# Optimization experiments

Hardware: AMD Instinct MI355X
Metric: run time of the kernel (lower is better)

The kernel has to match this reference:

```python
import jax, jax.numpy as jnp
import numpy as np

D_MODEL = 1024
HEADS = 16
D_K = D_MODEL // HEADS
NEG_INF = -1e10


def setup_inputs() -> dict:
    key = jax.random.key(0)
    ks = jax.random.split(key, 10)
    n, s = 2, 2048
    inp = {
        "value": jax.random.normal(ks[0], (n, s, D_MODEL), dtype=jnp.float32),
        "key": jax.random.normal(ks[1], (n, s, D_MODEL), dtype=jnp.float32),
        "query": jax.random.normal(ks[2], (n, s, D_MODEL), dtype=jnp.float32),
        "mask": jax.random.randint(ks[3], (n, 1, s, s), 0, 2, dtype=jnp.int32),
        # torch.nn.Linear weights are [out, in]; y = x @ W.T (+ b)
        "Wq": jax.random.normal(ks[4], (D_MODEL, D_MODEL), dtype=jnp.float32) * (D_MODEL ** -0.5),
        "Wk": jax.random.normal(ks[5], (D_MODEL, D_MODEL), dtype=jnp.float32) * (D_MODEL ** -0.5),
        "Wv": jax.random.normal(ks[6], (D_MODEL, D_MODEL), dtype=jnp.float32) * (D_MODEL ** -0.5),
        "Wo": jax.random.normal(ks[7], (D_MODEL, D_MODEL), dtype=jnp.float32) * (D_MODEL ** -0.5),
        "bo": jax.random.normal(ks[8], (D_MODEL,), dtype=jnp.float32) * 0.01,
    }
    return inp


def reference(value, key, query, mask, Wq, Wk, Wv, Wo, bo):
    n, q_len, _ = query.shape
    # projections (Linear, no bias): x @ W.T
    q = (query @ Wq.T).reshape(n, q_len, HEADS, D_K)
    k = (key @ Wk.T).reshape(n, key.shape[1], HEADS, D_K)
    v = (value @ Wv.T).reshape(n, value.shape[1], HEADS, D_K)
    scores = jnp.einsum('nqhd,nkhd->nhqk', q, k)  # [n,h,q,k]
    scores = jnp.where(mask == 0, jnp.float32(NEG_INF), scores)
    attn = jax.nn.softmax(scores / jnp.sqrt(jnp.float32(D_K)), axis=-1)
    out = jnp.einsum('nhql,nlhd->nqhd', attn, v).reshape(n, q_len, D_MODEL)
    return out @ Wo.T + bo
```

## Files before the change

kernel.cpp:

```cpp
#include <hip/hip_runtime.h>
#include <hip/hip_bf16.h>
#include <stdint.h>

#define SEQ     2048
#define NBATCH  2
#define DMODEL  1024
#define NH      16
#define DKH     64

typedef __bf16 bf16;
typedef __attribute__((ext_vector_type(8))) __bf16 bf16x8;
typedef __attribute__((ext_vector_type(4))) __bf16 bf16x4;
typedef __attribute__((ext_vector_type(4))) float  f32x4;

static __device__ __forceinline__ f32x4 mfma16(bf16x8 a, bf16x8 b, f32x4 c) {
    return __builtin_amdgcn_mfma_f32_16x16x32_bf16(a, b, c, 0, 0, 0);
}

#define PL32SWAP(a, b) asm("v_permlane32_swap_b32 %0, %1" : "+v"(a), "+v"(b))
#define PL16SWAP(a, b) asm("v_permlane16_swap_b32 %0, %1" : "+v"(a), "+v"(b))

__global__ __launch_bounds__(256) void cvt_all_k(const float* __restrict__ q,
                                                 const float* __restrict__ k,
                                                 const float* __restrict__ v,
                                                 const float* __restrict__ wq,
                                                 const float* __restrict__ wk,
                                                 const float* __restrict__ wv,
                                                 const float* __restrict__ wo,
                                                 const int* __restrict__ mask,
                                                 bf16* __restrict__ qb, bf16* __restrict__ kb,
                                                 bf16* __restrict__ vb, bf16* __restrict__ wqb,
                                                 bf16* __restrict__ wkb, bf16* __restrict__ wvb,
                                                 bf16* __restrict__ wob,
                                                 unsigned long long* __restrict__ mbits) {
    if (blockIdx.y == 7) {
        const int nwords = NBATCH * SEQ * (SEQ / 64);
        int wave  = (blockIdx.x * blockDim.x + threadIdx.x) >> 6;
        int lane  = threadIdx.x & 63;
        int nwtot = (gridDim.x * blockDim.x) >> 6;
        for (int w = wave; w < nwords; w += nwtot) {
            int m = mask[(size_t)w * 64 + lane];
            unsigned long long b = __ballot(m != 0);
            if (lane == 0) mbits[w] = b;
        }
        return;
    }
    const float* src; bf16* dst; int n4;
    const int NX4 = (NBATCH * SEQ * DMODEL) / 4, NW4 = (DMODEL * DMODEL) / 4;
    switch (blockIdx.y) {
        case 0: src = q;  dst = qb;  n4 = NX4; break;
        case 1: src = k;  dst = kb;  n4 = NX4; break;
        case 2: src = v;  dst = vb;  n4 = NX4; break;
        case 3: src = wq; dst = wqb; n4 = NW4; break;
        case 4: src = wk; dst = wkb; n4 = NW4; break;
        case 5: src = wv; dst = wvb; n4 = NW4; break;
        default: src = wo; dst = wob; n4 = NW4; break;
    }
    int stride = gridDim.x * blockDim.x;
    for (int i = blockIdx.x * blockDim.x + threadIdx.x; i < n4; i += stride) {
        f32x4 f = ((const f32x4*)src)[i];
        bf16x4 o;
#pragma unroll
        for (int j = 0; j < 4; j++) o[j] = (bf16)f[j];
        ((bf16x4*)dst)[i] = o;
    }
}

__global__ __launch_bounds__(256) void qkv_gemm(const bf16* __restrict__ Xq,
                                                const bf16* __restrict__ Xk,
                                                const bf16* __restrict__ Xv,
                                                const bf16* __restrict__ Wq,
                                                const bf16* __restrict__ Wk,
                                                const bf16* __restrict__ Wv,
                                                bf16* __restrict__ Qo,
                                                bf16* __restrict__ Ko,
                                                bf16* __restrict__ Vto) {
    __shared__ bf16 As[128 * 32], Bs[128 * 32];
    const int z = blockIdx.z;
    const bf16* A = (z == 0) ? Xq : (z == 1) ? Xk : Xv;
    const bf16* W = (z == 0) ? Wq : (z == 1) ? Wk : Wv;
    const int bm = blockIdx.x * 128, bn = blockIdx.y * 128;
    const int tid = threadIdx.x, wave = tid >> 6, lane = tid & 63;
    const int wm = wave >> 1, wn = wave & 1, lo = lane & 15, hi = lane >> 4;

    const int r0 = wave * 32 + (lane >> 2);
    const int c8 = (lane & 3) * 8;
    const bf16* Ag = A + (size_t)(bm + r0) * DMODEL + c8;
    const bf16* Bg = W + (size_t)(bn + r0) * DMODEL + c8;
    bf16* lA = &As[wave * 1024 + (lane >> 2) * 32 + (lane & 3) * 8];
    bf16* lB = &Bs[wave * 1024 + (lane >> 2) * 32 + (lane & 3) * 8];

    f32x4 acc[4][4];
#pragma unroll
    for (int i = 0; i < 4; i++)
#pragma unroll
        for (int j = 0; j < 4; j++) acc[i][j] = 0.0f;

    bf16x8 ra0 = *(const bf16x8*)(Ag);
    bf16x8 ra1 = *(const bf16x8*)(Ag + (size_t)16 * DMODEL);
    bf16x8 rb0 = *(const bf16x8*)(Bg);
    bf16x8 rb1 = *(const bf16x8*)(Bg + (size_t)16 * DMODEL);

#pragma unroll 1
    for (int k0 = 0; k0 < DMODEL; k0 += 32) {
        __syncthreads();
        *(bf16x8*)lA         = ra0;
        *(bf16x8*)(lA + 512) = ra1;
        *(bf16x8*)lB         = rb0;
        *(bf16x8*)(lB + 512) = rb1;
        if (k0 + 32 < DMODEL) {
            ra0 = *(const bf16x8*)(Ag + k0 + 32);
            ra1 = *(const bf16x8*)(Ag + k0 + 32 + (size_t)16 * DMODEL);
            rb0 = *(const bf16x8*)(Bg + k0 + 32);
            rb1 = *(const bf16x8*)(Bg + k0 + 32 + (size_t)16 * DMODEL);
        }
        __syncthreads();

        bf16x8 a[4], b[4];
#pragma unroll
        for (int t = 0; t < 4; t++) {
            a[t] = *(const bf16x8*)&As[(wm * 64 + t * 16 + lo) * 32 + hi * 8];
            b[t] = *(const bf16x8*)&Bs[(wn * 64 + t * 16 + lo) * 32 + hi * 8];
        }
        if (z < 2) {
#pragma unroll
            for (int tm = 0; tm < 4; tm++)
#pragma unroll
                for (int tn = 0; tn < 4; tn++)
                    acc[tm][tn] = mfma16(a[tm], b[tn], acc[tm][tn]);
        } else {
#pragma unroll
            for (int tm = 0; tm < 4; tm++)
#pragma unroll
                for (int tn = 0; tn < 4; tn++)
                    acc[tm][tn] = mfma16(b[tn], a[tm], acc[tm][tn]);
        }
    }

    if (z < 2) {
        bf16* O = (z == 0) ? Qo : Ko;
        const float qscale = (z == 0) ? 0.18033688f : 1.0f;
#pragma unroll
        for (int tm = 0; tm < 4; tm++)
#pragma unroll
            for (int tn = 0; tn < 4; tn++)
#pragma unroll
                for (int r = 0; r < 4; r++) {
                    int m = bm + wm * 64 + tm * 16 + hi * 4 + r;
                    int o = bn + wn * 64 + tn * 16 + lo;
                    int nidx = m >> 11, sq = m & 2047;
                    int hh = o >> 6, d = o & 63;
                    O[(((size_t)nidx * NH + hh) * SEQ + sq) * DKH + d] = (bf16)(acc[tm][tn][r] * qscale);
                }
    } else {
#pragma unroll
        for (int tm = 0; tm < 4; tm++)
#pragma unroll
            for (int tn = 0; tn < 4; tn++)
#pragma unroll
                for (int r = 0; r < 4; r++) {
                    int o = bn + wn * 64 + tn * 16 + hi * 4 + r;
                    int m = bm + wm * 64 + tm * 16 + lo;
                    int nidx = m >> 11, sq = m & 2047;
                    int hh = o >> 6, d = o & 63;
                    Vto[(((size_t)nidx * NH + hh) * DKH + d) * SEQ + sq] = (bf16)acc[tm][tn][r];
                }
    }
}

__global__ __launch_bounds__(256, 4) void attn_k(const bf16* __restrict__ Q,
                                                 const bf16* __restrict__ K,
                                                 const bf16* __restrict__ Vt,
                                                 const unsigned long long* __restrict__ mbits,
                                                 bf16* __restrict__ Op0,
                                                 bf16* __restrict__ Op1,
                                                 float* __restrict__ Lp,
                                                 int ksrange) {
    __shared__ bf16 Ks[64 * 72];
    __shared__ bf16 Vs[64 * 72];

    const int bid = blockIdx.x;
    const int xcd = bid & 7, j = bid >> 3;
    const int hd = xcd * 4 + (j & 3);
    const int qb = (j >> 2) & 15;
    const int ks = j >> 6;
    const int n = hd >> 4, h = hd & 15;

    const int tid = threadIdx.x, wave = tid >> 6, lane = tid & 63;
    const int lo = lane & 15, hi = lane >> 4;

    const size_t headoff = (size_t)hd * SEQ * DKH;
    const bf16* Qh = Q + headoff;
    const bf16* Kh = K + headoff;
    const bf16* Vh = Vt + headoff;

    const int qrowA = qb * 128 + wave * 16 + lo;
    const int qrowB = qrowA + 64;
    const bf16x8 aq0A = *(const bf16x8*)(Qh + (size_t)qrowA * DKH + hi * 8);
    const bf16x8 aq1A = *(const bf16x8*)(Qh + (size_t)qrowA * DKH + 32 + hi * 8);
    const bf16x8 aq0B = *(const bf16x8*)(Qh + (size_t)qrowB * DKH + hi * 8);
    const bf16x8 aq1B = *(const bf16x8*)(Qh + (size_t)qrowB * DKH + 32 + hi * 8);

    bf16x8 ones;
#pragma unroll
    for (int i = 0; i < 8; i++) ones[i] = (bf16)1.0f;

    f32x4 oaccA[4], oaccB[4];
#pragma unroll
    for (int t = 0; t < 4; t++) { oaccA[t] = 0.0f; oaccB[t] = 0.0f; }
    f32x4 laccA; laccA = 0.0f;
    f32x4 laccB; laccB = 0.0f;

    const unsigned long long* mbqA = mbits + ((size_t)n * SEQ + qrowA) * (SEQ / 64);
    const unsigned long long* mbqB = mbits + ((size_t)n * SEQ + qrowB) * (SEQ / 64);

    const int kbeg = ks * ksrange, kend = kbeg + ksrange;

    const int srow = tid >> 3, sseg = tid & 7;
    const bf16* Kg = Kh + (size_t)srow * DKH + sseg * 8;
    const bf16* Vg = Vh + (size_t)srow * SEQ + sseg * 8;

    bf16x8 rk0 = *(const bf16x8*)(Kg + (size_t)kbeg * DKH);
    bf16x8 rk1 = *(const bf16x8*)(Kg + (size_t)(kbeg + 32) * DKH);
    bf16x8 rv0 = *(const bf16x8*)(Vg + kbeg);
    bf16x8 rv1 = *(const bf16x8*)(Vg + (size_t)32 * SEQ + kbeg);
    unsigned long long wmA = mbqA[kbeg >> 6];
    unsigned long long wmB = mbqB[kbeg >> 6];
    unsigned long long wmnA = 0, wmnB = 0;

    union FragU { uint32_t u[4]; bf16x8 v; };

#pragma unroll 1
    for (int k0 = kbeg; k0 < kend; k0 += 64) {
        __syncthreads();
        *(bf16x8*)&Ks[srow * 72 + sseg * 8]        = rk0;
        *(bf16x8*)&Ks[(srow + 32) * 72 + sseg * 8] = rk1;
        *(bf16x8*)&Vs[srow * 72 + sseg * 8]        = rv0;
        *(bf16x8*)&Vs[(srow + 32) * 72 + sseg * 8] = rv1;
        if (k0 + 64 < kend) {
            rk0 = *(const bf16x8*)(Kg + (size_t)(k0 + 64) * DKH);
            rk1 = *(const bf16x8*)(Kg + (size_t)(k0 + 96) * DKH);
            rv0 = *(const bf16x8*)(Vg + k0 + 64);
            rv1 = *(const bf16x8*)(Vg + (size_t)32 * SEQ + k0 + 64);
            wmnA = mbqA[(k0 >> 6) + 1];
            wmnB = mbqB[(k0 >> 6) + 1];
        }
        __syncthreads();

        unsigned wloA = (unsigned)(wmA >> (hi * 4));
        unsigned whiA = (unsigned)(wmA >> (hi * 4 + 32));
        unsigned wloB = (unsigned)(wmB >> (hi * 4));
        unsigned whiB = (unsigned)(wmB >> (hi * 4 + 32));
        uint32_t pkA[4][2], pkB[4][2];
#pragma unroll
        for (int tn = 0; tn < 4; tn++) {
            const int kr = (tn * 16 + lo) * 72;
            bf16x8 b0 = *(const bf16x8*)&Ks[kr + hi * 8];
            bf16x8 b1 = *(const bf16x8*)&Ks[kr + 32 + hi * 8];
            f32x4 zA; zA = 0.0f;
            zA = mfma16(b0, aq0A, zA);
            zA = mfma16(b1, aq1A, zA);
            f32x4 zB; zB = 0.0f;
            zB = mfma16(b0, aq0B, zB);
            zB = mfma16(b1, aq1B, zB);
            unsigned wsA = ((tn < 2) ? wloA : whiA) >> ((tn & 1) * 16);
            unsigned wsB = ((tn < 2) ? wloB : whiB) >> ((tn & 1) * 16);
            float pvA[4], pvB[4];
#pragma unroll
            for (int r = 0; r < 4; r++) {
                float eA = __builtin_amdgcn_exp2f(zA[r]);
                pvA[r] = ((wsA >> r) & 1u) ? eA : 0.0f;
                float eB = __builtin_amdgcn_exp2f(zB[r]);
                pvB[r] = ((wsB >> r) & 1u) ? eB : 0.0f;
            }
            asm("v_cvt_pk_bf16_f32 %0, %1, %2" : "=v"(pkA[tn][0]) : "v"(pvA[0]), "v"(pvA[1]));
            asm("v_cvt_pk_bf16_f32 %0, %1, %2" : "=v"(pkA[tn][1]) : "v"(pvA[2]), "v"(pvA[3]));
            asm("v_cvt_pk_bf16_f32 %0, %1, %2" : "=v"(pkB[tn][0]) : "v"(pvB[0]), "v"(pvB[1]));
            asm("v_cvt_pk_bf16_f32 %0, %1, %2" : "=v"(pkB[tn][1]) : "v"(pvB[2]), "v"(pvB[3]));
        }
        wmA = wmnA;
        wmB = wmnB;

        bf16x8 ap0A, ap1A, ap0B, ap1B;
        {
            uint32_t d00 = pkA[0][0], d02 = pkA[1][0];
            PL32SWAP(d00, d02); PL16SWAP(d00, d02);
            uint32_t d01 = pkA[0][1], d03 = pkA[1][1];
            PL32SWAP(d01, d03); PL16SWAP(d01, d03);
            uint32_t d10 = pkA[2][0], d12 = pkA[3][0];
            PL32SWAP(d10, d12); PL16SWAP(d10, d12);
            uint32_t d11 = pkA[2][1], d13 = pkA[3][1];
            PL32SWAP(d11, d13); PL16SWAP(d11, d13);
            FragU f0, f1;
            f0.u[0] = d00; f0.u[1] = d01; f0.u[2] = d02; f0.u[3] = d03;
            f1.u[0] = d10; f1.u[1] = d11; f1.u[2] = d12; f1.u[3] = d13;
            ap0A = f0.v; ap1A = f1.v;
        }
        {
            uint32_t d00 = pkB[0][0], d02 = pkB[1][0];
            PL32SWAP(d00, d02); PL16SWAP(d00, d02);
            uint32_t d01 = pkB[0][1], d03 = pkB[1][1];
            PL32SWAP(d01, d03); PL16SWAP(d01, d03);
            uint32_t d10 = pkB[2][0], d12 = pkB[3][0];
            PL32SWAP(d10, d12); PL16SWAP(d10, d12);
            uint32_t d11 = pkB[2][1], d13 = pkB[3][1];
            PL32SWAP(d11, d13); PL16SWAP(d11, d13);
            FragU f0, f1;
            f0.u[0] = d00; f0.u[1] = d01; f0.u[2] = d02; f0.u[3] = d03;
            f1.u[0] = d10; f1.u[1] = d11; f1.u[2] = d12; f1.u[3] = d13;
            ap0B = f0.v; ap1B = f1.v;
        }

#pragma unroll
        for (int td = 0; td < 4; td++) {
            bf16x8 b0 = *(const bf16x8*)&Vs[(td * 16 + lo) * 72 + hi * 8];
            bf16x8 b1 = *(const bf16x8*)&Vs[(td * 16 + lo) * 72 + 32 + hi * 8];
            oaccA[td] = mfma16(ap0A, b0, oaccA[td]);
            oaccA[td] = mfma16(ap1A, b1, oaccA[td]);
            oaccB[td] = mfma16(ap0B, b0, oaccB[td]);
            oaccB[td] = mfma16(ap1B, b1, oaccB[td]);
        }
        laccA = mfma16(ap0A, ones, laccA);
        laccA = mfma16(ap1A, ones, laccA);
        laccB = mfma16(ap0B, ones, laccB);
        laccB = mfma16(ap1B, ones, laccB);
    }

    bf16* Op = ks ? Op1 : Op0;
#pragma unroll
    for (int td = 0; td < 4; td++)
#pragma unroll
        for (int r = 0; r < 4; r++) {
            int qA = qb * 128 + wave * 16 + hi * 4 + r;
            int qB = qA + 64;
            int d = td * 16 + lo;
            Op[((size_t)n * SEQ + qA) * DMODEL + h * 64 + d] = (bf16)oaccA[td][r];
            Op[((size_t)n * SEQ + qB) * DMODEL + h * 64 + d] = (bf16)oaccB[td][r];
        }
    if (lo == 0) {
#pragma unroll
        for (int r = 0; r < 4; r++) {
            int qA = qb * 128 + wave * 16 + hi * 4 + r;
            int qB = qA + 64;
            size_t base = (size_t)ks * (NBATCH * NH * SEQ) + ((size_t)(n * NH + h) * SEQ);
            Lp[base + qA] = laccA[r];
            Lp[base + qB] = laccB[r];
        }
    }
}

__global__ __launch_bounds__(256) void out_gemm(const bf16* __restrict__ o0,
                                                const bf16* __restrict__ o1,
                                                const float* __restrict__ lp,
                                                const bf16* __restrict__ W,
                                                const float* __restrict__ bias,
                                                float* __restrict__ Out) {
    __shared__ bf16 As[128 * 32], Bs[128 * 32];
    const int bm = blockIdx.x * 128, bn = blockIdx.y * 128;
    const int tid = threadIdx.x, wave = tid >> 6, lane = tid & 63;
    const int wm = wave >> 1, wn = wave & 1, lo = lane & 15, hi = lane >> 4;

    const int r0 = wave * 32 + (lane >> 2);
    const int c8 = (lane & 3) * 8;
    const int m1 = bm + r0, m2 = m1 + 16;
    const size_t aoff1 = (size_t)m1 * DMODEL + c8;
    const size_t aoff2 = (size_t)m2 * DMODEL + c8;
    const bf16* Bg = W + (size_t)(bn + r0) * DMODEL + c8;
    const int NL = NBATCH * NH * SEQ;
    const int li1b = (m1 >> 11) * (NH * SEQ) + (m1 & 2047);
    const int li2b = (m2 >> 11) * (NH * SEQ) + (m2 & 2047);
    bf16* lA = &As[wave * 1024 + (lane >> 2) * 32 + (lane & 3) * 8];
    bf16* lB = &Bs[wave * 1024 + (lane >> 2) * 32 + (lane & 3) * 8];

    f32x4 acc[4][4];
#pragma unroll
    for (int i = 0; i < 4; i++)
#pragma unroll
        for (int j = 0; j < 4; j++) acc[i][j] = 0.0f;

    bf16x8 px0 = *(const bf16x8*)(o0 + aoff1);
    bf16x8 py0 = *(const bf16x8*)(o1 + aoff1);
    bf16x8 px1 = *(const bf16x8*)(o0 + aoff2);
    bf16x8 py1 = *(const bf16x8*)(o1 + aoff2);
    bf16x8 pb0 = *(const bf16x8*)(Bg);
    bf16x8 pb1 = *(const bf16x8*)(Bg + (size_t)16 * DMODEL);
    float pl1a = lp[li1b], pl1b = lp[NL + li1b];
    float pl2a = lp[li2b], pl2b = lp[NL + li2b];

#pragma unroll 1
    for (int k0 = 0; k0 < DMODEL; k0 += 32) {
        __syncthreads();
        float rl1 = 1.0f / (pl1a + pl1b);
        float rl2 = 1.0f / (pl2a + pl2b);
        bf16x8 wa0, wa1;
#pragma unroll
        for (int jj = 0; jj < 8; jj++) {
            wa0[jj] = (bf16)(((float)px0[jj] + (float)py0[jj]) * rl1);
            wa1[jj] = (bf16)(((float)px1[jj] + (float)py1[jj]) * rl2);
        }
        *(bf16x8*)lA         = wa0;
        *(bf16x8*)(lA + 512) = wa1;
        *(bf16x8*)lB         = pb0;
        *(bf16x8*)(lB + 512) = pb1;
        if (k0 + 32 < DMODEL) {
            int h = (k0 + 32) >> 6;
            px0 = *(const bf16x8*)(o0 + aoff1 + k0 + 32);
            py0 = *(const bf16x8*)(o1 + aoff1 + k0 + 32);
            px1 = *(const bf16x8*)(o0 + aoff2 + k0 + 32);
            py1 = *(const bf16x8*)(o1 + aoff2 + k0 + 32);
            pb0 = *(const bf16x8*)(Bg + k0 + 32);
            pb1 = *(const bf16x8*)(Bg + k0 + 32 + (size_t)16 * DMODEL);
            int li1 = li1b + h * SEQ, li2 = li2b + h * SEQ;
            pl1a = lp[li1]; pl1b = lp[NL + li1];
            pl2a = lp[li2]; pl2b = lp[NL + li2];
        }
        __syncthreads();

        bf16x8 a[4], b[4];
#pragma unroll
        for (int t = 0; t < 4; t++) {
            a[t] = *(const bf16x8*)&As[(wm * 64 + t * 16 + lo) * 32 + hi * 8];
            b[t] = *(const bf16x8*)&Bs[(wn * 64 + t * 16 + lo) * 32 + hi * 8];
        }
#pragma unroll
        for (int tm = 0; tm < 4; tm++)
#pragma unroll
            for (int tn = 0; tn < 4; tn++)
                acc[tm][tn] = mfma16(a[tm], b[tn], acc[tm][tn]);
    }

#pragma unroll
    for (int tm = 0; tm < 4; tm++)
#pragma unroll
        for (int tn = 0; tn < 4; tn++) {
            int o = bn + wn * 64 + tn * 16 + lo;
            float bv = bias[o];
#pragma unroll
            for (int r = 0; r < 4; r++) {
                int m = bm + wm * 64 + tm * 16 + hi * 4 + r;
                Out[(size_t)m * DMODEL + o] = acc[tm][tn][r] + bv;
            }
        }
}

extern "C" void kernel_launch(void* const* d_in, const int* in_sizes, int n_in,
                              void* d_out, int out_size, void* d_ws, size_t ws_size,
                              hipStream_t stream) {
    const float* value = (const float*)d_in[0];
    const float* key   = (const float*)d_in[1];
    const float* query = (const float*)d_in[2];
    const int*   mask  = (const int*)d_in[3];
    const float* Wq    = (const float*)d_in[4];
    const float* Wk    = (const float*)d_in[5];
    const float* Wv    = (const float*)d_in[6];
    const float* Wo    = (const float*)d_in[7];
    const float* bo    = (const float*)d_in[8];
    float* out = (float*)d_out;

    char* ws = (char*)d_ws;
    bf16* Qws = (bf16*)(ws);
    bf16* Kws = (bf16*)(ws + (8u  << 20));
    bf16* Vt  = (bf16*)(ws + (16u << 20));
    bf16* Xqb = (bf16*)(ws + (24u << 20));
    bf16* Xkb = (bf16*)(ws + (32u << 20));
    bf16* Xvb = (bf16*)(ws + (40u << 20));
    bf16* Wqb = (bf16*)(ws + (48u << 20));
    bf16* Wkb = (bf16*)(ws + (50u << 20));
    bf16* Wvb = (bf16*)(ws + (52u << 20));
    bf16* Wob = (bf16*)(ws + (54u << 20));
    unsigned long long* mbits = (unsigned long long*)(ws + (56u << 20));
    bf16*  Op0 = Xqb;
    bf16*  Op1 = Xkb;
    float* Lp  = (float*)Wqb;

    const int  ksn     = 2;
    const int  ksrange = SEQ / ksn;
    const int  attn_grid = 32 * 16 * ksn;

    cvt_all_k<<<dim3(1024, 8), 256, 0, stream>>>(query, key, value, Wq, Wk, Wv, Wo, mask,
                                                 Xqb, Xkb, Xvb, Wqb, Wkb, Wvb, Wob, mbits);
    qkv_gemm<<<dim3(32, 8, 3), 256, 0, stream>>>(Xqb, Xkb, Xvb, Wqb, Wkb, Wvb, Qws, Kws, Vt);
    attn_k<<<attn_grid, 256, 0, stream>>>(Qws, Kws, Vt, mbits, Op0, Op1, Lp, ksrange);
    out_gemm<<<dim3(32, 8), 256, 0, stream>>>(Op0, Op1, Lp, Wob, bo, out);
}
```

Measured before the change: 273.6 us.

## Fuse activation fp32-to-bf16 conversion into QKV GEMM and double attention key tile

The separate conversion pass over query/key/value is removed. The QKV GEMM now loads fp32 activations directly and converts them to bf16 in registers before the LDS store, which avoids writing and re-reading a bf16 copy of the activations. Separately, the attention kernel now stages 128 keys per iteration (two 64-key sub-tiles) instead of 64, halving the number of barrier/LDS-fill rounds at the cost of more LDS per block, which may lower occupancy. The GEMM A-tile loads double in bytes, since fp32 activations are now re-read by every column block.

```diff
diff --git a/kernel.cpp b/kernel.cpp
--- a/kernel.cpp
+++ b/kernel.cpp
@@ -20,20 +20,17 @@
 #define PL32SWAP(a, b) asm("v_permlane32_swap_b32 %0, %1" : "+v"(a), "+v"(b))
 #define PL16SWAP(a, b) asm("v_permlane16_swap_b32 %0, %1" : "+v"(a), "+v"(b))
 
-__global__ __launch_bounds__(256) void cvt_all_k(const float* __restrict__ q,
-                                                 const float* __restrict__ k,
-                                                 const float* __restrict__ v,
-                                                 const float* __restrict__ wq,
+__global__ __launch_bounds__(256) void cvt_all_k(const float* __restrict__ wq,
                                                  const float* __restrict__ wk,
                                                  const float* __restrict__ wv,
                                                  const float* __restrict__ wo,
                                                  const int* __restrict__ mask,
-                                                 bf16* __restrict__ qb, bf16* __restrict__ kb,
-                                                 bf16* __restrict__ vb, bf16* __restrict__ wqb,
-                                                 bf16* __restrict__ wkb, bf16* __restrict__ wvb,
+                                                 bf16* __restrict__ wqb,
+                                                 bf16* __restrict__ wkb,
+                                                 bf16* __restrict__ wvb,
                                                  bf16* __restrict__ wob,
                                                  unsigned long long* __restrict__ mbits) {
-    if (blockIdx.y == 7) {
+    if (blockIdx.y == 4) {
         const int nwords = NBATCH * SEQ * (SEQ / 64);
         int wave  = (blockIdx.x * blockDim.x + threadIdx.x) >> 6;
         int lane  = threadIdx.x & 63;
@@ -45,19 +42,16 @@
         }
         return;
     }
-    const float* src; bf16* dst; int n4;
-    const int NX4 = (NBATCH * SEQ * DMODEL) / 4, NW4 = (DMODEL * DMODEL) / 4;
+    const float* src; bf16* dst;
     switch (blockIdx.y) {
-        case 0: src = q;  dst = qb;  n4 = NX4; break;
-        case 1: src = k;  dst = kb;  n4 = NX4; break;
-        case 2: src = v;  dst = vb;  n4 = NX4; break;
-        case 3: src = wq; dst = wqb; n4 = NW4; break;
-        case 4: src = wk; dst = wkb; n4 = NW4; break;
-        case 5: src = wv; dst = wvb; n4 = NW4; break;
-        default: src = wo; dst = wob; n4 = NW4; break;
-    }
+        case 0: src = wq; dst = wqb; break;
+        case 1: src = wk; dst = wkb; break;
+        case 2: src = wv; dst = wvb; break;
+        default: src = wo; dst = wob; break;
+    }
+    const int NW4 = (DMODEL * DMODEL) / 4;
     int stride = gridDim.x * blockDim.x;
-    for (int i = blockIdx.x * blockDim.x + threadIdx.x; i < n4; i += stride) {
+    for (int i = blockIdx.x * blockDim.x + threadIdx.x; i < NW4; i += stride) {
         f32x4 f = ((const f32x4*)src)[i];
         bf16x4 o;
 #pragma unroll
@@ -66,9 +60,9 @@
     }
 }
 
-__global__ __launch_bounds__(256) void qkv_gemm(const bf16* __restrict__ Xq,
-                                                const bf16* __restrict__ Xk,
-                                                const bf16* __restrict__ Xv,
+__global__ __launch_bounds__(256) void qkv_gemm(const float* __restrict__ Xq,
+                                                const float* __restrict__ Xk,
+                                                const float* __restrict__ Xv,
                                                 const bf16* __restrict__ Wq,
                                                 const bf16* __restrict__ Wk,
                                                 const bf16* __restrict__ Wv,
@@ -77,16 +71,16 @@
                                                 bf16* __restrict__ Vto) {
     __shared__ bf16 As[128 * 32], Bs[128 * 32];
     const int z = blockIdx.z;
-    const bf16* A = (z == 0) ? Xq : (z == 1) ? Xk : Xv;
-    const bf16* W = (z == 0) ? Wq : (z == 1) ? Wk : Wv;
+    const float* A = (z == 0) ? Xq : (z == 1) ? Xk : Xv;
+    const bf16*  W = (z == 0) ? Wq : (z == 1) ? Wk : Wv;
     const int bm = blockIdx.x * 128, bn = blockIdx.y * 128;
     const int tid = threadIdx.x, wave = tid >> 6, lane = tid & 63;
     const int wm = wave >> 1, wn = wave & 1, lo = lane & 15, hi = lane >> 4;
 
     const int r0 = wave * 32 + (lane >> 2);
     const int c8 = (lane & 3) * 8;
-    const bf16* Ag = A + (size_t)(bm + r0) * DMODEL + c8;
-    const bf16* Bg = W + (size_t)(bn + r0) * DMODEL + c8;
+    const float* Ag = A + (size_t)(bm + r0) * DMODEL + c8;
+    const bf16*  Bg = W + (size_t)(bn + r0) * DMODEL + c8;
     bf16* lA = &As[wave * 1024 + (lane >> 2) * 32 + (lane & 3) * 8];
     bf16* lB = &Bs[wave * 1024 + (lane >> 2) * 32 + (lane & 3) * 8];
 
@@ -96,21 +90,31 @@
 #pragma unroll
         for (int j = 0; j < 4; j++) acc[i][j] = 0.0f;
 
-    bf16x8 ra0 = *(const bf16x8*)(Ag);
-    bf16x8 ra1 = *(const bf16x8*)(Ag + (size_t)16 * DMODEL);
+    f32x4 fa0 = *(const f32x4*)(Ag);
+    f32x4 fa1 = *(const f32x4*)(Ag + 4);
+    f32x4 fa2 = *(const f32x4*)(Ag + (size_t)16 * DMODEL);
+    f32x4 fa3 = *(const f32x4*)(Ag + (size_t)16 * DMODEL + 4);
     bf16x8 rb0 = *(const bf16x8*)(Bg);
     bf16x8 rb1 = *(const bf16x8*)(Bg + (size_t)16 * DMODEL);
 
 #pragma unroll 1
     for (int k0 = 0; k0 < DMODEL; k0 += 32) {
         __syncthreads();
-        *(bf16x8*)lA         = ra0;
-        *(bf16x8*)(lA + 512) = ra1;
+        bf16x8 wa0, wa1;
+#pragma unroll
+        for (int j = 0; j < 4; j++) {
+            wa0[j] = (bf16)fa0[j]; wa0[4 + j] = (bf16)fa1[j];
+            wa1[j] = (bf16)fa2[j]; wa1[4 + j] = (bf16)fa3[j];
+        }
+        *(bf16x8*)lA         = wa0;
+        *(bf16x8*)(lA + 512) = wa1;
         *(bf16x8*)lB         = rb0;
         *(bf16x8*)(lB + 512) = rb1;
         if (k0 + 32 < DMODEL) {
-            ra0 = *(const bf16x8*)(Ag + k0 + 32);
-            ra1 = *(const bf16x8*)(Ag + k0 + 32 + (size_t)16 * DMODEL);
+            fa0 = *(const f32x4*)(Ag + k0 + 32);
+            fa1 = *(const f32x4*)(Ag + k0 + 36);
+            fa2 = *(const f32x4*)(Ag + k0 + 32 + (size_t)16 * DMODEL);
+            fa3 = *(const f32x4*)(Ag + k0 + 36 + (size_t)16 * DMODEL);
             rb0 = *(const bf16x8*)(Bg + k0 + 32);
             rb1 = *(const bf16x8*)(Bg + k0 + 32 + (size_t)16 * DMODEL);
         }
@@ -176,8 +180,8 @@
                                                  bf16* __restrict__ Op1,
                                                  float* __restrict__ Lp,
                                                  int ksrange) {
-    __shared__ bf16 Ks[64 * 72];
-    __shared__ bf16 Vs[64 * 72];
+    __shared__ bf16 Ks[128 * 72];
+    __shared__ bf16 Vs[64 * 136];
 
     const int bid = blockIdx.x;
     const int xcd = bid & 7, j = bid >> 3;
@@ -220,33 +224,21 @@
     const bf16* Kg = Kh + (size_t)srow * DKH + sseg * 8;
     const bf16* Vg = Vh + (size_t)srow * SEQ + sseg * 8;
 
-    bf16x8 rk0 = *(const bf16x8*)(Kg + (size_t)kbeg * DKH);
+    bf16x8 rk0 = *(const bf16x8*)(Kg + (size_t)(kbeg)      * DKH);
     bf16x8 rk1 = *(const bf16x8*)(Kg + (size_t)(kbeg + 32) * DKH);
+    bf16x8 rk2 = *(const bf16x8*)(Kg + (size_t)(kbeg + 64) * DKH);
+    bf16x8 rk3 = *(const bf16x8*)(Kg + (size_t)(kbeg + 96) * DKH);
     bf16x8 rv0 = *(const bf16x8*)(Vg + kbeg);
     bf16x8 rv1 = *(const bf16x8*)(Vg + (size_t)32 * SEQ + kbeg);
-    unsigned long long wmA = mbqA[kbeg >> 6];
-    unsigned long long wmB = mbqB[kbeg >> 6];
-    unsigned long long wmnA = 0, wmnB = 0;
+    bf16x8 rv2 = *(const bf16x8*)(Vg + kbeg + 64);
+    bf16x8 rv3 = *(const bf16x8*)(Vg + (size_t)32 * SEQ + kbeg + 64);
+    unsigned long long wmA0 = mbqA[(kbeg >> 6)], wmA1 = mbqA[(kbeg >> 6) + 1];
+    unsigned long long wmB0 = mbqB[(kbeg >> 6)], wmB1 = mbqB[(kbeg >> 6) + 1];
+    unsigned long long wmnA0 = 0, wmnA1 = 0, wmnB0 = 0, wmnB1 = 0;
 
     union FragU { uint32_t u[4]; bf16x8 v; };
 
-#pragma unroll 1
-    for (int k0 = kbeg; k0 < kend; k0 += 64) {
-        __syncthreads();
-        *(bf16x8*)&Ks[srow * 72 + sseg * 8]        = rk0;
-        *(bf16x8*)&Ks[(srow + 32) * 72 + sseg * 8] = rk1;
-        *(bf16x8*)&Vs[srow * 72 + sseg * 8]        = rv0;
-        *(bf16x8*)&Vs[(srow + 32) * 72 + sseg * 8] = rv1;
-        if (k0 + 64 < kend) {
-            rk0 = *(const bf16x8*)(Kg + (size_t)(k0 + 64) * DKH);
-            rk1 = *(const bf16x8*)(Kg + (size_t)(k0 + 96) * DKH);
-            rv0 = *(const bf16x8*)(Vg + k0 + 64);
-            rv1 = *(const bf16x8*)(Vg + (size_t)32 * SEQ + k0 + 64);
-            wmnA = mbqA[(k0 >> 6) + 1];
-            wmnB = mbqB[(k0 >> 6) + 1];
-        }
-        __syncthreads();
-
+    auto tile = [&](int koff, unsigned long long wmA, unsigned long long wmB) {
         unsigned wloA = (unsigned)(wmA >> (hi * 4));
         unsigned whiA = (unsigned)(wmA >> (hi * 4 + 32));
         unsigned wloB = (unsigned)(wmB >> (hi * 4));
@@ -254,7 +246,7 @@
         uint32_t pkA[4][2], pkB[4][2];
 #pragma unroll
         for (int tn = 0; tn < 4; tn++) {
-            const int kr = (tn * 16 + lo) * 72;
+            const int kr = (koff + tn * 16 + lo) * 72;
             bf16x8 b0 = *(const bf16x8*)&Ks[kr + hi * 8];
             bf16x8 b1 = *(const bf16x8*)&Ks[kr + 32 + hi * 8];
             f32x4 zA; zA = 0.0f;
@@ -278,8 +270,6 @@
             asm("v_cvt_pk_bf16_f32 %0, %1, %2" : "=v"(pkB[tn][0]) : "v"(pvB[0]), "v"(pvB[1]));
             asm("v_cvt_pk_bf16_f32 %0, %1, %2" : "=v"(pkB[tn][1]) : "v"(pvB[2]), "v"(pvB[3]));
         }
-        wmA = wmnA;
-        wmB = wmnB;
 
         bf16x8 ap0A, ap1A, ap0B, ap1B;
         {
@@ -313,8 +303,8 @@
 
 #pragma unroll
         for (int td = 0; td < 4; td++) {
-            bf16x8 b0 = *(const bf16x8*)&Vs[(td * 16 + lo) * 72 + hi * 8];
-            bf16x8 b1 = *(const bf16x8*)&Vs[(td * 16 + lo) * 72 + 32 + hi * 8];
+            bf16x8 b0 = *(const bf16x8*)&Vs[(td * 16 + lo) * 136 + koff + hi * 8];
+            bf16x8 b1 = *(const bf16x8*)&Vs[(td * 16 + lo) * 136 + koff + 32 + hi * 8];
             oaccA[td] = mfma16(ap0A, b0, oaccA[td]);
             oaccA[td] = mfma16(ap1A, b1, oaccA[td]);
             oaccB[td] = mfma16(ap0B, b0, oaccB[td]);
@@ -324,6 +314,38 @@
         laccA = mfma16(ap1A, ones, laccA);
         laccB = mfma16(ap0B, ones, laccB);
         laccB = mfma16(ap1B, ones, laccB);
+    };
+
+#pragma unroll 1
+    for (int k0 = kbeg; k0 < kend; k0 += 128) {
+        __syncthreads();
+        *(bf16x8*)&Ks[(srow)      * 72 + sseg * 8] = rk0;
+        *(bf16x8*)&Ks[(srow + 32) * 72 + sseg * 8] = rk1;
+        *(bf16x8*)&Ks[(srow + 64) * 72 + sseg * 8] = rk2;
+        *(bf16x8*)&Ks[(srow + 96) * 72 + sseg * 8] = rk3;
+        *(bf16x8*)&Vs[(srow)      * 136 + sseg * 8]      = rv0;
+        *(bf16x8*)&Vs[(srow + 32) * 136 + sseg * 8]      = rv1;
+        *(bf16x8*)&Vs[(srow)      * 136 + 64 + sseg * 8] = rv2;
+        *(bf16x8*)&Vs[(srow + 32) * 136 + 64 + sseg * 8] = rv3;
+        if (k0 + 128 < kend) {
+            rk0 = *(const bf16x8*)(Kg + (size_t)(k0 + 128) * DKH);
+            rk1 = *(const bf16x8*)(Kg + (size_t)(k0 + 160) * DKH);
+            rk2 = *(const bf16x8*)(Kg + (size_t)(k0 + 192) * DKH);
+            rk3 = *(const bf16x8*)(Kg + (size_t)(k0 + 224) * DKH);
+            rv0 = *(const bf16x8*)(Vg + k0 + 128);
+            rv1 = *(const bf16x8*)(Vg + (size_t)32 * SEQ + k0 + 128);
+            rv2 = *(const bf16x8*)(Vg + k0 + 192);
+            rv3 = *(const bf16x8*)(Vg + (size_t)32 * SEQ + k0 + 192);
+            wmnA0 = mbqA[(k0 >> 6) + 2]; wmnA1 = mbqA[(k0 >> 6) + 3];
+            wmnB0 = mbqB[(k0 >> 6) + 2]; wmnB1 = mbqB[(k0 >> 6) + 3];
+        }
+        __syncthreads();
+
+        tile(0,  wmA0, wmB0);
+        tile(64, wmA1, wmB1);
+
+        wmA0 = wmnA0; wmA1 = wmnA1;
+        wmB0 = wmnB0; wmB1 = wmnB1;
     }
 
     bf16* Op = ks ? Op1 : Op0;
@@ -461,25 +483,22 @@
     bf16* Qws = (bf16*)(ws);
     bf16* Kws = (bf16*)(ws + (8u  << 20));
     bf16* Vt  = (bf16*)(ws + (16u << 20));
-    bf16* Xqb = (bf16*)(ws + (24u << 20));
-    bf16* Xkb = (bf16*)(ws + (32u << 20));
-    bf16* Xvb = (bf16*)(ws + (40u << 20));
+    bf16* Op0 = (bf16*)(ws + (24u << 20));
+    bf16* Op1 = (bf16*)(ws + (32u << 20));
     bf16* Wqb = (bf16*)(ws + (48u << 20));
     bf16* Wkb = (bf16*)(ws + (50u << 20));
     bf16* Wvb = (bf16*)(ws + (52u << 20));
     bf16* Wob = (bf16*)(ws + (54u << 20));
     unsigned long long* mbits = (unsigned long long*)(ws + (56u << 20));
-    bf16*  Op0 = Xqb;
-    bf16*  Op1 = Xkb;
     float* Lp  = (float*)Wqb;
 
     const int  ksn     = 2;
     const int  ksrange = SEQ / ksn;
     const int  attn_grid = 32 * 16 * ksn;
 
-    cvt_all_k<<<dim3(1024, 8), 256, 0, stream>>>(query, key, value, Wq, Wk, Wv, Wo, mask,
-                                                 Xqb, Xkb, Xvb, Wqb, Wkb, Wvb, Wob, mbits);
-    qkv_gemm<<<dim3(32, 8, 3), 256, 0, stream>>>(Xqb, Xkb, Xvb, Wqb, Wkb, Wvb, Qws, Kws, Vt);
+    cvt_all_k<<<dim3(1024, 5), 256, 0, stream>>>(Wq, Wk, Wv, Wo, mask,
+                                                 Wqb, Wkb, Wvb, Wob, mbits);
+    qkv_gemm<<<dim3(32, 8, 3), 256, 0, stream>>>(query, key, value, Wqb, Wkb, Wvb, Qws, Kws, Vt);
     attn_k<<<attn_grid, 256, 0, stream>>>(Qws, Kws, Vt, mbits, Op0, Op1, Lp, ksrange);
     out_gemm<<<dim3(32, 8), 256, 0, stream>>>(Op0, Op1, Lp, Wob, bo, out);
 }
```

Result: slower. 312.0 us (+14.0%).
